# Kernel tuning notes

Measured on AMD Instinct MI355X. Metric: run time of the kernel, lower is better.

Reference implementation:

```python
import jax, jax.numpy as jnp
import numpy as np

F_SIZE = 256
GF_REDUCE = 0x1D  # low byte of galois' default primitive polynomial 0x11D for GF(2^8)


def _gf256_mul_table() -> np.ndarray:
    """Full 256x256 GF(2^8) multiplication table (poly x^8+x^4+x^3+x^2+1 = 0x11D),
    matching galois.GF(2**8) multiplication, built by Russian-peasant multiply."""
    a = np.broadcast_to(np.arange(F_SIZE, dtype=np.uint16)[:, None], (F_SIZE, F_SIZE)).copy()
    b = np.broadcast_to(np.arange(F_SIZE, dtype=np.uint16)[None, :], (F_SIZE, F_SIZE)).copy()
    res = np.zeros((F_SIZE, F_SIZE), dtype=np.uint16)
    for _ in range(8):
        res ^= np.where(b & 1, a, 0).astype(np.uint16)
        b >>= 1
        hi = a & 0x80
        a = (a << 1) & 0xFF
        a ^= np.where(hi, GF_REDUCE, 0).astype(np.uint16)
    return res.astype(np.int32)


def _xor_reduce_last(x: jnp.ndarray) -> jnp.ndarray:
    # associative tree XOR-fold over the last axis (replaces the python for-loop fold)
    return jax.lax.reduce(x, np.int32(0), jax.lax.bitwise_xor, (x.ndim - 1,))


def setup_inputs() -> dict:
    key = jax.random.key(0)
    k_m, k_s, k_P = jax.random.split(key, 3)
    B, K, N = 32, 16, 256
    m = jax.random.randint(k_m, (B, K), 0, F_SIZE, dtype=jnp.int32)
    s = jax.random.randint(k_s, (B, N), 0, F_SIZE, dtype=jnp.int32)
    P = jax.random.randint(k_P, (K, N, N), 0, F_SIZE, dtype=jnp.int32)
    table = jnp.asarray(_gf256_mul_table())  # [256,256] int32
    return {"m": m, "s": s, "P": P, "table": table}


def reference(m, s, P, table):
    # m: [B,K] int32, s: [B,N] int32, P: [K,N,N] int32, table: [256,256] int32
    # s_times_P[b,i,j] = XOR_l  s[b,l] * P[i,j,l]   (GF(256) mat-vec per check i)
    prod1 = table[s[:, None, None, :], P[None, :, :, :]]          # [B,K,N,N]
    s_times_P = _xor_reduce_last(prod1)                            # [B,K,N]
    # m_check[b,i] = (XOR_j  s_times_P[b,i,j] * s[b,j]) - m[b,i]  i.e. s^T P_i s - m
    prod2 = table[s_times_P, s[:, None, :]]                        # [B,K,N]
    m_check = _xor_reduce_last(prod2) - m                          # [B,K]
    return jnp.maximum(1 - m_check.sum(-1), 0)                     # relu(1 - sum) -> [B]
```

## Files before the change

### kernel.cpp

```cpp
#include <hip/hip_runtime.h>
#include <stdint.h>

enum { B_ = 32, K_ = 16, N_ = 256 };

#define WS_NEED 4096

#define M4 0x01010101u

__device__ __forceinline__ uint32_t pack4i(int4 v) {
    return (uint32_t)(v.x & 255) | ((uint32_t)(v.y & 255) << 8) |
           ((uint32_t)(v.z & 255) << 16) | ((uint32_t)(v.w & 255) << 24);
}

__global__ __launch_bounds__(512) void gf_main6(const int* __restrict__ s32,
                                                const int* __restrict__ P32,
                                                int* __restrict__ part) {
    __shared__ uint32_t ptile[128 * 64];
    __shared__ __align__(16) uint8_t cvb[4][2048];
    __shared__ uint2 ct_lds[4][256];
    __shared__ uint32_t xch[4][2][128];
    __shared__ uint32_t wr[8];

    const int bid = blockIdx.x;
    const int k = bid & 15, nh = (bid >> 4) & 1, bq = bid >> 5;
    const int tid = threadIdx.x;

    {
        const int j = tid & 255;
#pragma unroll
        for (int e = 0; e < 2; ++e) {
            const int bbx = (tid >> 8) + 2 * e;
            uint32_t c = (uint32_t)s32[(bq * 4 + bbx) * 256 + j] & 255u;
            uint32_t A = 0, Bw = 0;
#pragma unroll
            for (int u = 0; u < 4; ++u) {
                A |= c << (8 * u);
                c = ((c << 1) & 255u) ^ ((c >> 7) * 29u);
            }
#pragma unroll
            for (int u = 0; u < 4; ++u) {
                Bw |= c << (8 * u);
                c = ((c << 1) & 255u) ^ ((c >> 7) * 29u);
            }
            uint32_t by[8];
#pragma unroll
            for (int r = 0; r < 8; ++r) {
                uint32_t t = (A >> r) & M4;
                uint32_t lo = (t | (t >> 7) | (t >> 14) | (t >> 21)) & 15u;
                uint32_t u2 = (Bw >> r) & M4;
                uint32_t hi = (u2 | (u2 >> 7) | (u2 >> 14) | (u2 >> 21)) & 15u;
                by[r] = lo | (hi << 4);
                cvb[bbx][r * 256 + j] = (uint8_t)by[r];
            }
            uint2 ct;
            ct.x = by[0] | (by[1] << 8) | (by[2] << 16) | (by[3] << 24);
            ct.y = by[4] | (by[5] << 8) | (by[6] << 16) | (by[7] << 24);
            ct_lds[bbx][j] = ct;
        }
    }

    const int4* praw = (const int4*)P32 + (size_t)k * 16384 + nh * 8192;
#pragma unroll 8
    for (int it = 0; it < 16; ++it) {
        const int g = tid + 512 * it;
        uint32_t w = pack4i(praw[g]);
        const int n = g >> 6, ihi = (g >> 2) & 15, wq = g & 3;
        ptile[(n << 6) + ((ihi ^ (n & 15)) << 2) + wq] = w;
    }
    __syncthreads();

    {
        const int bh = __builtin_amdgcn_readfirstlane(tid >> 6);
        const int bb = bh >> 1, h = bh & 1;
        const int nl = tid & 63;
        const int nx = nl & 15;
        const uint4* cvq = (const uint4*)cvb[bb];
        const uint32_t* prow0 = &ptile[nl << 6];
        const uint32_t* prow1 = &ptile[(nl + 64) << 6];
        uint32_t xa0 = 0, xa1 = 0, xa2 = 0, xa3 = 0, xa4 = 0, xa5 = 0, xa6 = 0, xa7 = 0;
        uint32_t xb0 = 0, xb1 = 0, xb2 = 0, xb3 = 0, xb4 = 0, xb5 = 0, xb6 = 0, xb7 = 0;
#pragma unroll 4
        for (int ii = 0; ii < 8; ++ii) {
            const int i = 8 * h + ii;
            const int slot = (i ^ nx) << 2;
            uint4 p0 = *(const uint4*)(prow0 + slot);
            uint4 p1 = *(const uint4*)(prow1 + slot);
#define CACC(xa, xb, r)                                                       \
            {                                                                 \
                uint4 cc = cvq[(r) * 16 + i];                                 \
                xa ^= (cc.x & p0.x) ^ (cc.y & p0.y) ^ (cc.z & p0.z) ^ (cc.w & p0.w); \
                xb ^= (cc.x & p1.x) ^ (cc.y & p1.y) ^ (cc.z & p1.z) ^ (cc.w & p1.w); \
            }
            CACC(xa0, xb0, 0) CACC(xa1, xb1, 1) CACC(xa2, xb2, 2) CACC(xa3, xb3, 3)
            CACC(xa4, xb4, 4) CACC(xa5, xb5, 5) CACC(xa6, xb6, 6) CACC(xa7, xb7, 7)
#undef CACC
        }
        uint32_t pa = (uint32_t)(__popc(xa0) & 1) | ((uint32_t)(__popc(xa1) & 1) << 1) |
                      ((uint32_t)(__popc(xa2) & 1) << 2) | ((uint32_t)(__popc(xa3) & 1) << 3) |
                      ((uint32_t)(__popc(xa4) & 1) << 4) | ((uint32_t)(__popc(xa5) & 1) << 5) |
                      ((uint32_t)(__popc(xa6) & 1) << 6) | ((uint32_t)(__popc(xa7) & 1) << 7);
        uint32_t pb = (uint32_t)(__popc(xb0) & 1) | ((uint32_t)(__popc(xb1) & 1) << 1) |
                      ((uint32_t)(__popc(xb2) & 1) << 2) | ((uint32_t)(__popc(xb3) & 1) << 3) |
                      ((uint32_t)(__popc(xb4) & 1) << 4) | ((uint32_t)(__popc(xb5) & 1) << 5) |
                      ((uint32_t)(__popc(xb6) & 1) << 6) | ((uint32_t)(__popc(xb7) & 1) << 7);
        xch[bb][h][nl] = pa;
        xch[bb][h][nl + 64] = pb;
    }
    __syncthreads();

    {
        const int bb = tid >> 7, nl = tid & 127;
        uint32_t stP = xch[bb][0][nl] ^ xch[bb][1][nl];
        uint2 ct = ct_lds[bb][nh * 128 + nl];
        uint32_t prod = 0;
#pragma unroll
        for (int r = 0; r < 4; ++r)
            prod |= (uint32_t)(__popc(stP & ((ct.x >> (8 * r)) & 255u)) & 1) << r;
#pragma unroll
        for (int r = 0; r < 4; ++r)
            prod |= (uint32_t)(__popc(stP & ((ct.y >> (8 * r)) & 255u)) & 1) << (r + 4);

        uint32_t acc = prod;
#pragma unroll
        for (int off = 1; off < 64; off <<= 1) acc ^= __shfl_xor(acc, off, 64);
        if ((tid & 63) == 0) wr[tid >> 6] = acc;
    }
    __syncthreads();
    if (tid == 0) {
#pragma unroll
        for (int bb = 0; bb < 4; ++bb) {
            int pv = (int)(wr[2 * bb] ^ wr[2 * bb + 1]);
            part[(bq * 4 + bb) * 32 + k * 2 + nh] = pv;
        }
    }
}

__global__ __launch_bounds__(512) void gf_fin(const int* __restrict__ part,
                                              const int* __restrict__ m32,
                                              int* __restrict__ dout) {
    __shared__ int sd[512];
    const int t = threadIdx.x;
    sd[t] = (int)(((const uint32_t*)part)[2 * t] ^ ((const uint32_t*)part)[2 * t + 1]) - m32[t];
    __syncthreads();
    if (t < 32) {
        int s = 0;
#pragma unroll
        for (int kk = 0; kk < 16; ++kk) s += sd[t * 16 + kk];
        dout[t] = max(1 - s, 0);
    }
}

__global__ void prep_zero(int* __restrict__ out) {
    if (threadIdx.x < B_) out[threadIdx.x] = 0;
}
#define LK(sw, pw)                                                  \
    v ^= tbl[(((sw) & 255u) << 8) | ((pw) & 255u)];                 \
    v ^= tbl[((sw) & 0xFF00u) | (((pw) >> 8) & 255u)];              \
    v ^= tbl[(((sw) >> 8) & 0xFF00u) | (((pw) >> 16) & 255u)];      \
    v ^= tbl[(((sw) >> 16) & 0xFF00u) | ((pw) >> 24)];
__global__ __launch_bounds__(256) void gf_main_fb(const int* __restrict__ m,
                                                  const int* __restrict__ s32,
                                                  const int* __restrict__ P32,
                                                  const int* __restrict__ t32,
                                                  int* __restrict__ out) {
    __shared__ uint8_t tbl[65536];
    __shared__ uint8_t sb[256];
    __shared__ uint32_t wred[4];
    const int b = blockIdx.x >> 4, k = blockIdx.x & 15, tid = threadIdx.x;
    for (int i = tid; i < 16384; i += 256) {
        int4 v = ((const int4*)t32)[i];
        ((uint32_t*)tbl)[i] = pack4i(v);
    }
    if (tid < 64) {
        int4 v = ((const int4*)s32)[b * 64 + tid];
        ((uint32_t*)sb)[tid] = pack4i(v);
    }
    __syncthreads();
    uint32_t v = 0;
    const uint32_t* sw32 = (const uint32_t*)sb;
    const int4* prow32 = (const int4*)(P32 + ((size_t)k * N_ + tid) * N_);
#pragma unroll 4
    for (int j0 = 0; j0 < 64; j0 += 4) {
        uint32_t p0 = pack4i(prow32[j0]), p1 = pack4i(prow32[j0 + 1]);
        uint32_t p2 = pack4i(prow32[j0 + 2]), p3 = pack4i(prow32[j0 + 3]);
        uint32_t w0 = sw32[j0], w1 = sw32[j0 + 1], w2 = sw32[j0 + 2], w3 = sw32[j0 + 3];
        LK(w0, p0) LK(w1, p1) LK(w2, p2) LK(w3, p3)
    }
    uint32_t wv = tbl[(v << 8) | (uint32_t)sb[tid]];
#pragma unroll
    for (int off = 1; off < 64; off <<= 1) wv ^= __shfl_xor(wv, off, 64);
    if ((tid & 63) == 0) wred[tid >> 6] = wv;
    __syncthreads();
    if (tid == 0) {
        uint32_t x = wred[0] ^ wred[1] ^ wred[2] ^ wred[3];
        atomicAdd(&out[b], (int)x - m[b * K_ + k]);
    }
}
__global__ void gf_finish_fb(int* __restrict__ out) {
    if (threadIdx.x < B_) {
        int v = out[threadIdx.x];
        out[threadIdx.x] = max(1 - v, 0);
    }
}

extern "C" void kernel_launch(void* const* d_in, const int* in_sizes, int n_in,
                              void* d_out, int out_size, void* d_ws, size_t ws_size,
                              hipStream_t stream) {
    const int* m     = (const int*)d_in[0];
    const int* s     = (const int*)d_in[1];
    const int* P     = (const int*)d_in[2];
    const int* table = (const int*)d_in[3];
    int* out = (int*)d_out;

    if (ws_size >= (size_t)WS_NEED) {
        int* part = (int*)d_ws;
        gf_main6<<<256, 512, 0, stream>>>(s, P, part);
        gf_fin<<<1, 512, 0, stream>>>(part, m, out);
    } else {
        prep_zero<<<1, 64, 0, stream>>>(out);
        gf_main_fb<<<B_ * K_, 256, 0, stream>>>(m, s, P, table, out);
        gf_finish_fb<<<1, 64, 0, stream>>>(out);
    }
}
```

Measured before the change: 13.66 us.

## Prefetch P tile into registers early and split contraction four ways per row group

All sixteen global P loads are now issued into registers at kernel start, before the s-derived table construction, so the memory latency overlaps that compute. Byte packing switches to v_perm. The contraction is re-tiled so each thread handles 4 rows over 4 i-chunks instead of 2 rows over 8, which improves reuse of the cvb loads. The partial results are now combined by XOR across four slices. The cost is much higher register pressure (64 VGPRs for the prefetch plus 32 accumulators), which could hurt occupancy or cause spills.

```diff
diff --git a/kernel.cpp b/kernel.cpp
--- a/kernel.cpp
+++ b/kernel.cpp
@@ -12,18 +12,35 @@
            ((uint32_t)(v.z & 255) << 16) | ((uint32_t)(v.w & 255) << 24);
 }
 
-__global__ __launch_bounds__(512) void gf_main6(const int* __restrict__ s32,
+#if __has_builtin(__builtin_amdgcn_perm)
+__device__ __forceinline__ uint32_t pack4p(uint4 v) {
+    uint32_t lo = __builtin_amdgcn_perm(v.y, v.x, 0x0C0C0400u);
+    uint32_t hi = __builtin_amdgcn_perm(v.w, v.z, 0x04000C0Cu);
+    return lo | hi;
+}
+#else
+__device__ __forceinline__ uint32_t pack4p(uint4 v) {
+    return (v.x & 255u) | ((v.y & 255u) << 8) | ((v.z & 255u) << 16) | ((v.w & 255u) << 24);
+}
+#endif
+
+__global__ __launch_bounds__(512) void gf_main7(const int* __restrict__ s32,
                                                 const int* __restrict__ P32,
                                                 int* __restrict__ part) {
     __shared__ uint32_t ptile[128 * 64];
     __shared__ __align__(16) uint8_t cvb[4][2048];
     __shared__ uint2 ct_lds[4][256];
-    __shared__ uint32_t xch[4][2][128];
+    __shared__ uint32_t xch[4 * 4 * 128];
     __shared__ uint32_t wr[8];
 
     const int bid = blockIdx.x;
     const int k = bid & 15, nh = (bid >> 4) & 1, bq = bid >> 5;
     const int tid = threadIdx.x;
+
+    const uint4* praw = (const uint4*)P32 + (size_t)k * 16384 + (size_t)nh * 8192;
+    uint4 pr_[16];
+#pragma unroll
+    for (int it = 0; it < 16; ++it) pr_[it] = praw[tid + 512 * it];
 
     {
         const int j = tid & 255;
@@ -59,59 +76,65 @@
         }
     }
 
-    const int4* praw = (const int4*)P32 + (size_t)k * 16384 + nh * 8192;
-#pragma unroll 8
+#pragma unroll
     for (int it = 0; it < 16; ++it) {
         const int g = tid + 512 * it;
-        uint32_t w = pack4i(praw[g]);
+        uint32_t w = pack4p(pr_[it]);
         const int n = g >> 6, ihi = (g >> 2) & 15, wq = g & 3;
         ptile[(n << 6) + ((ihi ^ (n & 15)) << 2) + wq] = w;
     }
     __syncthreads();
 
     {
-        const int bh = __builtin_amdgcn_readfirstlane(tid >> 6);
-        const int bb = bh >> 1, h = bh & 1;
-        const int nl = tid & 63;
+        const int bb = __builtin_amdgcn_readfirstlane(tid >> 7);
+        const int iq = (tid >> 5) & 3;
+        const int nl = tid & 31;
         const int nx = nl & 15;
         const uint4* cvq = (const uint4*)cvb[bb];
         const uint32_t* prow0 = &ptile[nl << 6];
-        const uint32_t* prow1 = &ptile[(nl + 64) << 6];
-        uint32_t xa0 = 0, xa1 = 0, xa2 = 0, xa3 = 0, xa4 = 0, xa5 = 0, xa6 = 0, xa7 = 0;
-        uint32_t xb0 = 0, xb1 = 0, xb2 = 0, xb3 = 0, xb4 = 0, xb5 = 0, xb6 = 0, xb7 = 0;
-#pragma unroll 4
-        for (int ii = 0; ii < 8; ++ii) {
-            const int i = 8 * h + ii;
+        const uint32_t* prow1 = &ptile[(nl + 32) << 6];
+        const uint32_t* prow2 = &ptile[(nl + 64) << 6];
+        const uint32_t* prow3 = &ptile[(nl + 96) << 6];
+
+        uint32_t x0_[8] = {0,0,0,0,0,0,0,0};
+        uint32_t x1_[8] = {0,0,0,0,0,0,0,0};
+        uint32_t x2_[8] = {0,0,0,0,0,0,0,0};
+        uint32_t x3_[8] = {0,0,0,0,0,0,0,0};
+#pragma unroll
+        for (int ii = 0; ii < 4; ++ii) {
+            const int i = iq * 4 + ii;
             const int slot = (i ^ nx) << 2;
             uint4 p0 = *(const uint4*)(prow0 + slot);
             uint4 p1 = *(const uint4*)(prow1 + slot);
-#define CACC(xa, xb, r)                                                       \
-            {                                                                 \
-                uint4 cc = cvq[(r) * 16 + i];                                 \
-                xa ^= (cc.x & p0.x) ^ (cc.y & p0.y) ^ (cc.z & p0.z) ^ (cc.w & p0.w); \
-                xb ^= (cc.x & p1.x) ^ (cc.y & p1.y) ^ (cc.z & p1.z) ^ (cc.w & p1.w); \
-            }
-            CACC(xa0, xb0, 0) CACC(xa1, xb1, 1) CACC(xa2, xb2, 2) CACC(xa3, xb3, 3)
-            CACC(xa4, xb4, 4) CACC(xa5, xb5, 5) CACC(xa6, xb6, 6) CACC(xa7, xb7, 7)
-#undef CACC
+            uint4 p2 = *(const uint4*)(prow2 + slot);
+            uint4 p3 = *(const uint4*)(prow3 + slot);
+#pragma unroll
+            for (int r = 0; r < 8; ++r) {
+                uint4 cc = cvq[r * 16 + i];
+                x0_[r] ^= (cc.x & p0.x) ^ (cc.y & p0.y) ^ (cc.z & p0.z) ^ (cc.w & p0.w);
+                x1_[r] ^= (cc.x & p1.x) ^ (cc.y & p1.y) ^ (cc.z & p1.z) ^ (cc.w & p1.w);
+                x2_[r] ^= (cc.x & p2.x) ^ (cc.y & p2.y) ^ (cc.z & p2.z) ^ (cc.w & p2.w);
+                x3_[r] ^= (cc.x & p3.x) ^ (cc.y & p3.y) ^ (cc.z & p3.z) ^ (cc.w & p3.w);
+            }
         }
-        uint32_t pa = (uint32_t)(__popc(xa0) & 1) | ((uint32_t)(__popc(xa1) & 1) << 1) |
-                      ((uint32_t)(__popc(xa2) & 1) << 2) | ((uint32_t)(__popc(xa3) & 1) << 3) |
-                      ((uint32_t)(__popc(xa4) & 1) << 4) | ((uint32_t)(__popc(xa5) & 1) << 5) |
-                      ((uint32_t)(__popc(xa6) & 1) << 6) | ((uint32_t)(__popc(xa7) & 1) << 7);
-        uint32_t pb = (uint32_t)(__popc(xb0) & 1) | ((uint32_t)(__popc(xb1) & 1) << 1) |
-                      ((uint32_t)(__popc(xb2) & 1) << 2) | ((uint32_t)(__popc(xb3) & 1) << 3) |
-                      ((uint32_t)(__popc(xb4) & 1) << 4) | ((uint32_t)(__popc(xb5) & 1) << 5) |
-                      ((uint32_t)(__popc(xb6) & 1) << 6) | ((uint32_t)(__popc(xb7) & 1) << 7);
-        xch[bb][h][nl] = pa;
-        xch[bb][h][nl + 64] = pb;
+        const int xb = ((bb * 4 + iq) << 7) + nl;
+        uint32_t pb;
+#define EMIT(xa, rr)                                                           \
+        pb = (uint32_t)(__popc(xa[0]) & 1)        | ((uint32_t)(__popc(xa[1]) & 1) << 1) | \
+             ((uint32_t)(__popc(xa[2]) & 1) << 2) | ((uint32_t)(__popc(xa[3]) & 1) << 3) | \
+             ((uint32_t)(__popc(xa[4]) & 1) << 4) | ((uint32_t)(__popc(xa[5]) & 1) << 5) | \
+             ((uint32_t)(__popc(xa[6]) & 1) << 6) | ((uint32_t)(__popc(xa[7]) & 1) << 7); \
+        xch[xb + 32 * rr] = pb;
+        EMIT(x0_, 0) EMIT(x1_, 1) EMIT(x2_, 2) EMIT(x3_, 3)
+#undef EMIT
     }
     __syncthreads();
 
     {
-        const int bb = tid >> 7, nl = tid & 127;
-        uint32_t stP = xch[bb][0][nl] ^ xch[bb][1][nl];
-        uint2 ct = ct_lds[bb][nh * 128 + nl];
+        const int bb = tid >> 7, n2 = tid & 127;
+        uint32_t stP = xch[(bb * 4 + 0) * 128 + n2] ^ xch[(bb * 4 + 1) * 128 + n2] ^
+                       xch[(bb * 4 + 2) * 128 + n2] ^ xch[(bb * 4 + 3) * 128 + n2];
+        uint2 ct = ct_lds[bb][nh * 128 + n2];
         uint32_t prod = 0;
 #pragma unroll
         for (int r = 0; r < 4; ++r)
@@ -214,7 +237,7 @@
 
     if (ws_size >= (size_t)WS_NEED) {
         int* part = (int*)d_ws;
-        gf_main6<<<256, 512, 0, stream>>>(s, P, part);
+        gf_main7<<<256, 512, 0, stream>>>(s, P, part);
         gf_fin<<<1, 512, 0, stream>>>(part, m, out);
     } else {
         prep_zero<<<1, 64, 0, stream>>>(out);
```

New measurement: 13.48 us. Within noise of the previous version (-1.3%).
